# Optimization experiments

Measured on AMD Instinct MI355X. Metric: run time of the kernel, lower is better.

## Reference

```python
import jax, jax.numpy as jnp
import numpy as np
from jax.ops import segment_sum, segment_max

N_ROAD = 100000; E_ROAD = 400000
N_ZONE = 20000;  E_ZONE = 160000
D_ID = 64; D_ATTR = 16; H = 128; N_TYPES = 32


def setup_inputs():
    key = jax.random.key(0)
    ks = [jax.random.fold_in(key, i) for i in range(64)]
    it = iter(ks)
    p = lambda *s: jax.random.normal(next(it), s, jnp.float32) * 0.02
    inp = {
        'road_id_emb': p(N_ROAD, D_ID),
        'len_W': p(1, D_ATTR), 'len_b': p(D_ATTR),
        'type_emb': p(N_TYPES, D_ATTR),
        'lon_W': p(1, D_ATTR), 'lon_b': p(D_ATTR),
        'lat_W': p(1, D_ATTR), 'lat_b': p(D_ATTR),
        'road_attr_len': jax.random.normal(next(it), (N_ROAD,), jnp.float32),
        'road_attr_type': jax.random.randint(next(it), (N_ROAD,), 0, N_TYPES),
        'road_attr_lon': jax.random.normal(next(it), (N_ROAD,), jnp.float32),
        'road_attr_lat': jax.random.normal(next(it), (N_ROAD,), jnp.float32),
        'road_edge_index': jax.random.randint(next(it), (2, E_ROAD), 0, N_ROAD),
        'intersection_attr': jax.random.normal(next(it), (E_ROAD, 2), jnp.float32),
        'gat1_Wl': p(H, H), 'gat1_bl': p(H), 'gat1_Wr': p(H, H), 'gat1_br': p(H),
        'gat1_We': p(2, H), 'gat1_att': p(H), 'gat1_bias': p(H),
        'gat2_Wl': p(H, H), 'gat2_bl': p(H), 'gat2_Wr': p(H, H), 'gat2_br': p(H),
        'gat2_We': p(2, H), 'gat2_att': p(H), 'gat2_bias': p(H),
        'zone_id_emb': p(N_ZONE, H),
        'zone_edge_index': jax.random.randint(next(it), (2, E_ZONE), 0, N_ZONE),
        'zone_edge_weight': jax.random.uniform(next(it), (E_ZONE,), jnp.float32, 0.1, 1.0),
        'gcn1_W': p(H, H), 'gcn1_b': p(H),
        'gcn2_W': p(H, H), 'gcn2_b': p(H),
    }
    return inp


def gatv2_layer(x, src, dst, edge_attr, Wl, bl, Wr, br, We, att, bias):
    # GATv2Conv, heads=1, concat, negative_slope=0.2, add_self_loops with
    # fill_value='mean' for edge_attr (mean of incoming edge attrs per node).
    N = x.shape[0]
    ones = jnp.ones((src.shape[0],), x.dtype)
    cnt = segment_sum(ones, dst, num_segments=N)
    mean_ea = segment_sum(edge_attr, dst, num_segments=N) / jnp.maximum(cnt, 1.0)[:, None]
    loop = jnp.arange(N)
    src2 = jnp.concatenate([src, loop])
    dst2 = jnp.concatenate([dst, loop])
    ea2 = jnp.concatenate([edge_attr, mean_ea], axis=0)
    xl = x @ Wl + bl   # source transform (messages)
    xr = x @ Wr + br   # target transform
    e = jax.nn.leaky_relu(xl[src2] + xr[dst2] + ea2 @ We, 0.2)  # [E2, H]
    logits = e @ att  # [E2]
    m = jax.lax.stop_gradient(segment_max(logits, dst2, num_segments=N))
    ex = jnp.exp(logits - m[dst2])
    denom = segment_sum(ex, dst2, num_segments=N)
    alpha = ex / denom[dst2]
    out = segment_sum(alpha[:, None] * xl[src2], dst2, num_segments=N)
    return out + bias


def gcn_layer(x, src, dst, w, W, b):
    # GCNConv with add_self_loops (weight 1) and symmetric normalization.
    N = x.shape[0]
    loop = jnp.arange(N)
    src2 = jnp.concatenate([src, loop])
    dst2 = jnp.concatenate([dst, loop])
    w2 = jnp.concatenate([w, jnp.ones((N,), x.dtype)])
    deg = segment_sum(w2, dst2, num_segments=N)
    dinv = jnp.where(deg > 0, jax.lax.rsqrt(jnp.maximum(deg, 1e-12)), 0.0)
    norm = dinv[src2] * w2 * dinv[dst2]
    h = x @ W
    return segment_sum(norm[:, None] * h[src2], dst2, num_segments=N) + b


def reference(road_id_emb, len_W, len_b, type_emb, lon_W, lon_b, lat_W, lat_b,
              road_attr_len, road_attr_type, road_attr_lon, road_attr_lat,
              road_edge_index, intersection_attr,
              gat1_Wl, gat1_bl, gat1_Wr, gat1_br, gat1_We, gat1_att, gat1_bias,
              gat2_Wl, gat2_bl, gat2_Wr, gat2_br, gat2_We, gat2_att, gat2_bias,
              zone_id_emb, zone_edge_index, zone_edge_weight,
              gcn1_W, gcn1_b, gcn2_W, gcn2_b):
    # ---- road node features: id emb || len lin || type emb || lon lin || lat lin
    x = jnp.concatenate([
        road_id_emb,
        road_attr_len[:, None] @ len_W + len_b,
        type_emb[road_attr_type],
        road_attr_lon[:, None] @ lon_W + lon_b,
        road_attr_lat[:, None] @ lat_W + lat_b,
    ], axis=1)  # [N_ROAD, H]
    src, dst = road_edge_index[0], road_edge_index[1]
    h = jax.nn.relu(gatv2_layer(x, src, dst, intersection_attr,
                                gat1_Wl, gat1_bl, gat1_Wr, gat1_br, gat1_We, gat1_att, gat1_bias))
    road_out = gatv2_layer(h, src, dst, intersection_attr,
                           gat2_Wl, gat2_bl, gat2_Wr, gat2_br, gat2_We, gat2_att, gat2_bias)
    # ---- zone GCN over zone_id embedding table
    zsrc, zdst = zone_edge_index[0], zone_edge_index[1]
    zh = jax.nn.relu(gcn_layer(zone_id_emb, zsrc, zdst, zone_edge_weight, gcn1_W, gcn1_b))
    zone_out = gcn_layer(zh, zsrc, zdst, zone_edge_weight, gcn2_W, gcn2_b)
    return road_out, zone_out
```

## Files before the change

kernel.cpp:

```cpp
#include <hip/hip_runtime.h>
#include <math.h>


typedef __attribute__((ext_vector_type(8))) short bf16x8;
typedef __attribute__((ext_vector_type(4))) float f32x4;

static __device__ __forceinline__ unsigned short f2b(float f) {
  unsigned u = __float_as_uint(f);
  u = (u + 0x7FFFu + ((u >> 16) & 1u)) >> 16;
  return (unsigned short)u;
}
static __device__ __forceinline__ float b2f(unsigned short u) {
  return __uint_as_float(((unsigned)u) << 16);
}

__global__ __launch_bounds__(256) void wcast6(
    const float* __restrict__ W0, const float* __restrict__ W1, const float* __restrict__ W2,
    const float* __restrict__ W3, const float* __restrict__ W4, const float* __restrict__ W5,
    unsigned short* __restrict__ WT) {
  int b = blockIdx.x >> 6;
  int idx = (blockIdx.x & 63) * 256 + threadIdx.x;
  const float* W = (b == 0) ? W0 : (b == 1) ? W1 : (b == 2) ? W2 : (b == 3) ? W3 : (b == 4) ? W4 : W5;
  int n = idx >> 7, k = idx & 127;
  WT[b * 16384 + idx] = f2b(W[k * 128 + n]);
}


__global__ __launch_bounds__(256) void hist2(const int* __restrict__ dstR, int E,
                                             const int* __restrict__ dstZ, int EZ,
                                             int* __restrict__ histR, int* __restrict__ histZ) {
  int e = blockIdx.x * 256 + threadIdx.x;
  if (e < E) atomicAdd(histR + dstR[e], 1);
  else if (e - E < EZ) atomicAdd(histZ + dstZ[e - E], 1);
}

__global__ __launch_bounds__(256) void scan_local2(
    const int* __restrict__ inR, int* __restrict__ outR, int* __restrict__ bsumR, int nR, int nbR,
    const int* __restrict__ inZ, int* __restrict__ outZ, int* __restrict__ bsumZ, int nZ) {
  __shared__ int lds[256];
  const int* in; int* out; int* bsum; int n; int bid;
  if ((int)blockIdx.x < nbR) { in = inR; out = outR; bsum = bsumR; n = nR; bid = blockIdx.x; }
  else { in = inZ; out = outZ; bsum = bsumZ; n = nZ; bid = blockIdx.x - nbR; }
  int t = threadIdx.x;
  int base = bid * 1024 + t * 4;
  int v0 = base + 0 < n ? in[base + 0] : 0;
  int v1 = base + 1 < n ? in[base + 1] : 0;
  int v2 = base + 2 < n ? in[base + 2] : 0;
  int v3 = base + 3 < n ? in[base + 3] : 0;
  int s = v0 + v1 + v2 + v3;
  lds[t] = s;
  __syncthreads();
  for (int off = 1; off < 256; off <<= 1) {
    int x = (t >= off) ? lds[t - off] : 0;
    __syncthreads();
    if (t >= off) lds[t] += x;
    __syncthreads();
  }
  int excl = lds[t] - s;
  if (t == 255) bsum[bid] = lds[255];
  if (base + 0 < n) out[base + 0] = excl;
  if (base + 1 < n) out[base + 1] = excl + v0;
  if (base + 2 < n) out[base + 2] = excl + v0 + v1;
  if (base + 3 < n) out[base + 3] = excl + v0 + v1 + v2;
}

__global__ __launch_bounds__(256) void scan_bsum2(int* __restrict__ bsumR, int nbR,
                                                  int* __restrict__ bsumZ, int nbZ) {
  __shared__ int lds[256];
  int* bsum = blockIdx.x ? bsumZ : bsumR;
  int nb = blockIdx.x ? nbZ : nbR;
  int t = threadIdx.x;
  int v = (t < nb) ? bsum[t] : 0;
  lds[t] = v;
  __syncthreads();
  for (int off = 1; off < 256; off <<= 1) {
    int x = (t >= off) ? lds[t - off] : 0;
    __syncthreads();
    if (t >= off) lds[t] += x;
    __syncthreads();
  }
  if (t < nb) bsum[t] = lds[t] - v;
}

__global__ __launch_bounds__(256) void scan_add2(int* __restrict__ outR, const int* __restrict__ bsumR, int nR,
                                                 int* __restrict__ outZ, const int* __restrict__ bsumZ, int nZ) {
  int i = blockIdx.x * 256 + threadIdx.x;
  if (i < nR) outR[i] += bsumR[i >> 10];
  else if (i - nR < nZ) { int j = i - nR; outZ[j] += bsumZ[j >> 10]; }
}

__global__ __launch_bounds__(256) void scatter2(
    const int* __restrict__ srcR, const int* __restrict__ dstR, const float* __restrict__ ia,
    const int* __restrict__ rowstart, int* __restrict__ cursor,
    int* __restrict__ csr_src, float2* __restrict__ csr_ea, int E,
    const int* __restrict__ srcZ, const int* __restrict__ dstZ, const float* __restrict__ zw,
    const int* __restrict__ zrowstart, int* __restrict__ zcursor,
    int* __restrict__ zcsr_src, float* __restrict__ zcsr_w, int EZ) {
  int e = blockIdx.x * 256 + threadIdx.x;
  if (e < E) {
    int d = dstR[e];
    int idx = rowstart[d] + atomicAdd(cursor + d, 1);
    csr_src[idx] = srcR[e];
    csr_ea[idx] = make_float2(ia[2 * e], ia[2 * e + 1]);
  } else if (e - E < EZ) {
    int ez = e - E;
    int d = dstZ[ez];
    int idx = zrowstart[d] + atomicAdd(zcursor + d, 1);
    zcsr_src[idx] = srcZ[ez];
    zcsr_w[idx] = zw[ez];
  }
}

__global__ __launch_bounds__(256) void meanea_dinv_k(
    const int* __restrict__ rowstart, const int* __restrict__ hist,
    const float2* __restrict__ csr_ea, float2* __restrict__ mea, int N,
    const int* __restrict__ zrowstart, const int* __restrict__ zhist,
    const float* __restrict__ zcsr_w, float* __restrict__ dinv, int NZ) {
  int i = blockIdx.x * 256 + threadIdx.x;
  if (i < N) {
    int st = rowstart[i], deg = hist[i];
    float a = 0.f, b = 0.f;
    for (int k = 0; k < deg; ++k) {
      float2 v = csr_ea[st + k];
      a += v.x; b += v.y;
    }
    float c = deg > 0 ? 1.f / (float)deg : 0.f;
    mea[i] = make_float2(a * c, b * c);
  } else if (i - N < NZ) {
    int d = i - N;
    int st = zrowstart[d], deg = zhist[d];
    float s = 1.f;
    for (int k = 0; k < deg; ++k) s += zcsr_w[st + k];
    dinv[d] = rsqrtf(s);
  }
}

template <int DUAL>
__device__ __forceinline__ void gemm_core(
    unsigned short (*Xs)[136],
    const unsigned short* __restrict__ WlT, const unsigned short* __restrict__ WrT,
    const float* __restrict__ bl, const float* __restrict__ br,
    unsigned short* __restrict__ Yl, unsigned short* __restrict__ Yr,
    int row0, int N) {
  constexpr int MT = DUAL ? 4 : 2;
  int t = threadIdx.x;
  int w = t >> 6, lane = t & 63;
  int mb = DUAL ? 0 : (w >> 1) * 2;
  int ncol0 = (w & 1) * 64;
  const bool isR = DUAL && (w >> 1);
  const unsigned short* WTw = isR ? WrT : WlT;
  const float* bias = isR ? br : bl;
  int l15 = lane & 15, l4 = lane >> 4;

  bf16x8 b0[4], b1[4];
#pragma unroll
  for (int nt = 0; nt < 4; ++nt) {
    const unsigned short* p = WTw + (size_t)(ncol0 + nt * 16 + l15) * 128 + l4 * 8;
    b0[nt] = *reinterpret_cast<const bf16x8*>(p);
  }
  f32x4 acc[MT][4];
#pragma unroll
  for (int mt = 0; mt < MT; ++mt)
#pragma unroll
    for (int nt = 0; nt < 4; ++nt)
      acc[mt][nt] = (f32x4){0.f, 0.f, 0.f, 0.f};

#pragma unroll
  for (int ks = 0; ks < 4; ++ks) {
    bf16x8* bc = (ks & 1) ? b1 : b0;
    bf16x8* bn = (ks & 1) ? b0 : b1;
    if (ks < 3) {
#pragma unroll
      for (int nt = 0; nt < 4; ++nt) {
        const unsigned short* p = WTw + (size_t)(ncol0 + nt * 16 + l15) * 128 + (ks + 1) * 32 + l4 * 8;
        bn[nt] = *reinterpret_cast<const bf16x8*>(p);
      }
    }
    bf16x8 a[MT];
#pragma unroll
    for (int mt = 0; mt < MT; ++mt)
      a[mt] = *reinterpret_cast<const bf16x8*>(&Xs[(mb + mt) * 16 + l15][ks * 32 + l4 * 8]);
#pragma unroll
    for (int mt = 0; mt < MT; ++mt)
#pragma unroll
      for (int nt = 0; nt < 4; ++nt)
        acc[mt][nt] = __builtin_amdgcn_mfma_f32_16x16x32_bf16(bc[nt], a[mt], acc[mt][nt], 0, 0, 0);
  }

  const int passes = DUAL ? 2 : 1;
#pragma unroll
  for (int pass = 0; pass < passes; ++pass) {
    __syncthreads();
    if (!DUAL || (w >> 1) == pass) {
#pragma unroll
      for (int nt = 0; nt < 4; ++nt) {
        int c0 = ncol0 + nt * 16 + l4 * 4;
        float4 bv = make_float4(0.f, 0.f, 0.f, 0.f);
        if (bias) bv = *reinterpret_cast<const float4*>(bias + c0);
#pragma unroll
        for (int mt = 0; mt < MT; ++mt) {
          int rl = (mb + mt) * 16 + l15;
          ushort4 pk;
          pk.x = f2b(acc[mt][nt][0] + bv.x);
          pk.y = f2b(acc[mt][nt][1] + bv.y);
          pk.z = f2b(acc[mt][nt][2] + bv.z);
          pk.w = f2b(acc[mt][nt][3] + bv.w);
          *reinterpret_cast<ushort4*>(&Xs[rl][c0]) = pk;
        }
      }
    }
    __syncthreads();
    unsigned short* Yt = DUAL ? (pass ? Yr : Yl) : Yl;
#pragma unroll
    for (int q = 0; q < 4; ++q) {
      int lin = q * 256 + t;
      int r = lin >> 4, cc = (lin & 15) * 8;
      int row = row0 + r;
      if (row < N)
        *reinterpret_cast<bf16x8*>(Yt + (size_t)row * 128 + cc) =
            *reinterpret_cast<const bf16x8*>(&Xs[r][cc]);
    }
  }
}

template <int DUAL, int XBF>
__global__ __launch_bounds__(256) void gemm_mfma(
    const void* __restrict__ Xv,
    const unsigned short* __restrict__ WlT, const unsigned short* __restrict__ WrT,
    const float* __restrict__ bl, const float* __restrict__ br,
    unsigned short* __restrict__ Yl, unsigned short* __restrict__ Yr, int N) {
  __shared__ __align__(16) unsigned short Xs[64][136];
  int t = threadIdx.x;
  int row0 = blockIdx.x * 64;
  if (XBF) {
    const unsigned short* Xb = (const unsigned short*)Xv;
#pragma unroll
    for (int q = 0; q < 8; ++q) {
      int lin = q * 256 + t;
      int r = lin >> 5, kf = (lin & 31) * 4;
      int row = min(row0 + r, N - 1);
      *reinterpret_cast<ushort4*>(&Xs[r][kf]) =
          *reinterpret_cast<const ushort4*>(Xb + (size_t)row * 128 + kf);
    }
  } else {
    const float* Xf = (const float*)Xv;
#pragma unroll
    for (int q = 0; q < 8; ++q) {
      int lin = q * 256 + t;
      int r = lin >> 5, kf = (lin & 31) * 4;
      int row = min(row0 + r, N - 1);
      float4 xv = *reinterpret_cast<const float4*>(Xf + (size_t)row * 128 + kf);
      ushort4 pk;
      pk.x = f2b(xv.x); pk.y = f2b(xv.y); pk.z = f2b(xv.z); pk.w = f2b(xv.w);
      *reinterpret_cast<ushort4*>(&Xs[r][kf]) = pk;
    }
  }
  __syncthreads();
  gemm_core<DUAL>(Xs, WlT, WrT, bl, br, Yl, Yr, row0, N);
}

__global__ __launch_bounds__(256) void feat_gemm1(
    const float* __restrict__ id_emb, const float* __restrict__ lenW, const float* __restrict__ lenb,
    const float* __restrict__ type_emb, const float* __restrict__ lonW, const float* __restrict__ lonb,
    const float* __restrict__ latW, const float* __restrict__ latb,
    const float* __restrict__ alen, const int* __restrict__ atype,
    const float* __restrict__ alon, const float* __restrict__ alat,
    const unsigned short* __restrict__ WlT, const unsigned short* __restrict__ WrT,
    const float* __restrict__ bl, const float* __restrict__ br,
    unsigned short* __restrict__ Yl, unsigned short* __restrict__ Yr, int N) {
  __shared__ __align__(16) unsigned short Xs[64][136];
  int t = threadIdx.x;
  int row0 = blockIdx.x * 64;
#pragma unroll
  for (int q = 0; q < 8; ++q) {
    int lin = q * 256 + t;
    int r = lin >> 5, kf = (lin & 31) * 4;
    int row = min(row0 + r, N - 1);
    float v0, v1, v2, v3;
    if (kf < 64) {
      float4 e = *reinterpret_cast<const float4*>(id_emb + (size_t)row * 64 + kf);
      v0 = e.x; v1 = e.y; v2 = e.z; v3 = e.w;
    } else if (kf < 80) {
      float a = alen[row]; int j = kf - 64;
      v0 = a * lenW[j] + lenb[j]; v1 = a * lenW[j + 1] + lenb[j + 1];
      v2 = a * lenW[j + 2] + lenb[j + 2]; v3 = a * lenW[j + 3] + lenb[j + 3];
    } else if (kf < 96) {
      int ty = atype[row];
      float4 e = *reinterpret_cast<const float4*>(type_emb + ty * 16 + (kf - 80));
      v0 = e.x; v1 = e.y; v2 = e.z; v3 = e.w;
    } else if (kf < 112) {
      float a = alon[row]; int j = kf - 96;
      v0 = a * lonW[j] + lonb[j]; v1 = a * lonW[j + 1] + lonb[j + 1];
      v2 = a * lonW[j + 2] + lonb[j + 2]; v3 = a * lonW[j + 3] + lonb[j + 3];
    } else {
      float a = alat[row]; int j = kf - 112;
      v0 = a * latW[j] + latb[j]; v1 = a * latW[j + 1] + latb[j + 1];
      v2 = a * latW[j + 2] + latb[j + 2]; v3 = a * latW[j + 3] + latb[j + 3];
    }
    ushort4 pk;
    pk.x = f2b(v0); pk.y = f2b(v1); pk.z = f2b(v2); pk.w = f2b(v3);
    *reinterpret_cast<ushort4*>(&Xs[r][kf]) = pk;
  }
  __syncthreads();
  gemm_core<1>(Xs, WlT, WrT, bl, br, Yl, Yr, row0, N);
}

__device__ __forceinline__ float4 gat_one(
    const unsigned short* __restrict__ xl, float4 xr4,
    int d, int st, int deg, float2 me, int lane,
    const int* __restrict__ csr_src, const float2* __restrict__ csr_ea,
    float4 w0, float4 w1, float4 at) {
  float denom;
  float4 acc;
  {
    ushort4 av = *reinterpret_cast<const ushort4*>(xl + (size_t)d * 128 + lane * 4);
    float4 a;
    a.x = b2f(av.x); a.y = b2f(av.y); a.z = b2f(av.z); a.w = b2f(av.w);
    float4 v;
    v.x = a.x + xr4.x + me.x * w0.x + me.y * w1.x; v.x = v.x > 0.f ? v.x : 0.2f * v.x;
    v.y = a.y + xr4.y + me.x * w0.y + me.y * w1.y; v.y = v.y > 0.f ? v.y : 0.2f * v.y;
    v.z = a.z + xr4.z + me.x * w0.z + me.y * w1.z; v.z = v.z > 0.f ? v.z : 0.2f * v.z;
    v.w = a.w + xr4.w + me.x * w0.w + me.y * w1.w; v.w = v.w > 0.f ? v.w : 0.2f * v.w;
    float p = v.x * at.x + v.y * at.y + v.z * at.z + v.w * at.w;
#pragma unroll
    for (int off = 16; off; off >>= 1) p += __shfl_xor(p, off, 32);
    float wgt = __expf(p);
    denom = wgt;
    acc.x = wgt * a.x; acc.y = wgt * a.y; acc.z = wgt * a.z; acc.w = wgt * a.w;
  }
  for (int base = 0; base < deg; base += 32) {
    int rem = deg - base;
    int chunk = rem < 32 ? rem : 32;
    int k = st + base + lane;
    int sidx = 0;
    float2 eav = make_float2(0.f, 0.f);
    if (lane < chunk) { sidx = csr_src[k]; eav = csr_ea[k]; }
    auto edge = [&](ushort4 avv, int i) {
      float ea0 = __shfl(eav.x, i, 32);
      float ea1 = __shfl(eav.y, i, 32);
      float4 a;
      a.x = b2f(avv.x); a.y = b2f(avv.y); a.z = b2f(avv.z); a.w = b2f(avv.w);
      float4 v;
      v.x = a.x + xr4.x + ea0 * w0.x + ea1 * w1.x; v.x = v.x > 0.f ? v.x : 0.2f * v.x;
      v.y = a.y + xr4.y + ea0 * w0.y + ea1 * w1.y; v.y = v.y > 0.f ? v.y : 0.2f * v.y;
      v.z = a.z + xr4.z + ea0 * w0.z + ea1 * w1.z; v.z = v.z > 0.f ? v.z : 0.2f * v.z;
      v.w = a.w + xr4.w + ea0 * w0.w + ea1 * w1.w; v.w = v.w > 0.f ? v.w : 0.2f * v.w;
      float p = v.x * at.x + v.y * at.y + v.z * at.z + v.w * at.w;
#pragma unroll
      for (int off = 16; off; off >>= 1) p += __shfl_xor(p, off, 32);
      float wgt = __expf(p);
      denom += wgt;
      acc.x += wgt * a.x; acc.y += wgt * a.y; acc.z += wgt * a.z; acc.w += wgt * a.w;
    };
    for (int i0 = 0; i0 < chunk; i0 += 4) {
      int cnt = chunk - i0; if (cnt > 4) cnt = 4;
      int s0 = __shfl(sidx, i0 + 0, 32);
      int s1 = __shfl(sidx, i0 + 1, 32);
      int s2 = __shfl(sidx, i0 + 2, 32);
      int s3 = __shfl(sidx, i0 + 3, 32);
      ushort4 a0, a1, a2, a3;
      a0 = *reinterpret_cast<const ushort4*>(xl + (size_t)s0 * 128 + lane * 4);
      if (cnt > 1) a1 = *reinterpret_cast<const ushort4*>(xl + (size_t)s1 * 128 + lane * 4);
      if (cnt > 2) a2 = *reinterpret_cast<const ushort4*>(xl + (size_t)s2 * 128 + lane * 4);
      if (cnt > 3) a3 = *reinterpret_cast<const ushort4*>(xl + (size_t)s3 * 128 + lane * 4);
      edge(a0, i0 + 0);
      if (cnt > 1) edge(a1, i0 + 1);
      if (cnt > 2) edge(a2, i0 + 2);
      if (cnt > 3) edge(a3, i0 + 3);
    }
  }
  float inv = 1.f / denom;
  float4 o;
  o.x = acc.x * inv; o.y = acc.y * inv; o.z = acc.z * inv; o.w = acc.w * inv;
  return o;
}

template <int OUTBF>
__global__ __launch_bounds__(256) void gat_node(
    const unsigned short* __restrict__ xl, const unsigned short* __restrict__ xr,
    const int* __restrict__ rowstart, const int* __restrict__ hist,
    const int* __restrict__ csr_src, const float2* __restrict__ csr_ea,
    const float2* __restrict__ mean_ea,
    const float* __restrict__ We, const float* __restrict__ att, const float* __restrict__ bias,
    void* __restrict__ out, int N, int relu) {
  __shared__ float sW0[128], sW1[128], sAtt[128], sBias[128];
  int t = threadIdx.x;
  if (t < 128) { sW0[t] = We[t]; sW1[t] = We[128 + t]; }
  else { int j = t - 128; sAtt[j] = att[j]; sBias[j] = bias[j]; }
  __syncthreads();
  int grp = t >> 5, lane = t & 31;
  int d = blockIdx.x * 8 + grp;
  if (d >= N) return;
  float4 w0 = *reinterpret_cast<const float4*>(sW0 + lane * 4);
  float4 w1 = *reinterpret_cast<const float4*>(sW1 + lane * 4);
  float4 at = *reinterpret_cast<const float4*>(sAtt + lane * 4);
  float4 bv = *reinterpret_cast<const float4*>(sBias + lane * 4);
  ushort4 xrv = *reinterpret_cast<const ushort4*>(xr + (size_t)d * 128 + lane * 4);
  float4 xr4;
  xr4.x = b2f(xrv.x); xr4.y = b2f(xrv.y); xr4.z = b2f(xrv.z); xr4.w = b2f(xrv.w);
  float4 o = gat_one(xl, xr4, d, rowstart[d], hist[d], mean_ea[d], lane,
                     csr_src, csr_ea, w0, w1, at);
  o.x += bv.x; o.y += bv.y; o.z += bv.z; o.w += bv.w;
  if (relu) {
    o.x = fmaxf(o.x, 0.f); o.y = fmaxf(o.y, 0.f);
    o.z = fmaxf(o.z, 0.f); o.w = fmaxf(o.w, 0.f);
  }
  if (OUTBF) {
    ushort4 p4;
    p4.x = f2b(o.x); p4.y = f2b(o.y); p4.z = f2b(o.z); p4.w = f2b(o.w);
    *reinterpret_cast<ushort4*>((unsigned short*)out + (size_t)d * 128 + lane * 4) = p4;
  } else {
    *reinterpret_cast<float4*>((float*)out + (size_t)d * 128 + lane * 4) = o;
  }
}

__device__ __forceinline__ float4 gcn_one(
    const unsigned short* __restrict__ h, int d, int st, int deg, float dv, int lane,
    const int* __restrict__ csr_src, const float* __restrict__ csr_w,
    const float* __restrict__ dinv) {
  ushort4 hv = *reinterpret_cast<const ushort4*>(h + (size_t)d * 128 + lane * 4);
  float dv2 = dv * dv;
  float4 acc;
  acc.x = dv2 * b2f(hv.x); acc.y = dv2 * b2f(hv.y);
  acc.z = dv2 * b2f(hv.z); acc.w = dv2 * b2f(hv.w);
  for (int base = 0; base < deg; base += 32) {
    int rem = deg - base;
    int chunk = rem < 32 ? rem : 32;
    int k = st + base + lane;
    int sidx = 0;
    float wv = 0.f, dvs = 0.f;
    if (lane < chunk) {
      sidx = csr_src[k];
      wv = csr_w[k];
      dvs = dinv[sidx];
    }
    auto edge = [&](ushort4 avv, int i) {
      float coef = __shfl(dvs, i, 32) * __shfl(wv, i, 32) * dv;
      acc.x += coef * b2f(avv.x); acc.y += coef * b2f(avv.y);
      acc.z += coef * b2f(avv.z); acc.w += coef * b2f(avv.w);
    };
    for (int i0 = 0; i0 < chunk; i0 += 4) {
      int cnt = chunk - i0; if (cnt > 4) cnt = 4;
      int s0 = __shfl(sidx, i0 + 0, 32);
      int s1 = __shfl(sidx, i0 + 1, 32);
      int s2 = __shfl(sidx, i0 + 2, 32);
      int s3 = __shfl(sidx, i0 + 3, 32);
      ushort4 a0, a1, a2, a3;
      a0 = *reinterpret_cast<const ushort4*>(h + (size_t)s0 * 128 + lane * 4);
      if (cnt > 1) a1 = *reinterpret_cast<const ushort4*>(h + (size_t)s1 * 128 + lane * 4);
      if (cnt > 2) a2 = *reinterpret_cast<const ushort4*>(h + (size_t)s2 * 128 + lane * 4);
      if (cnt > 3) a3 = *reinterpret_cast<const ushort4*>(h + (size_t)s3 * 128 + lane * 4);
      edge(a0, i0 + 0);
      if (cnt > 1) edge(a1, i0 + 1);
      if (cnt > 2) edge(a2, i0 + 2);
      if (cnt > 3) edge(a3, i0 + 3);
    }
  }
  return acc;
}

template <int OUTBF>
__global__ __launch_bounds__(256) void gcn_node(const unsigned short* __restrict__ h,
                                                const int* __restrict__ rowstart,
                                                const int* __restrict__ hist, const int* __restrict__ csr_src,
                                                const float* __restrict__ csr_w, const float* __restrict__ dinv,
                                                const float* __restrict__ bias, void* __restrict__ out,
                                                int NZ, int relu) {
  int t = threadIdx.x, grp = t >> 5, lane = t & 31;
  int d = blockIdx.x * 8 + grp;
  if (d >= NZ) return;
  float4 acc = gcn_one(h, d, rowstart[d], hist[d], dinv[d], lane, csr_src, csr_w, dinv);
  float4 bv = *reinterpret_cast<const float4*>(bias + lane * 4);
  float4 o;
  o.x = acc.x + bv.x; o.y = acc.y + bv.y; o.z = acc.z + bv.z; o.w = acc.w + bv.w;
  if (relu) {
    o.x = fmaxf(o.x, 0.f); o.y = fmaxf(o.y, 0.f);
    o.z = fmaxf(o.z, 0.f); o.w = fmaxf(o.w, 0.f);
  }
  if (OUTBF) {
    ushort4 p4;
    p4.x = f2b(o.x); p4.y = f2b(o.y); p4.z = f2b(o.z); p4.w = f2b(o.w);
    *reinterpret_cast<ushort4*>((unsigned short*)out + (size_t)d * 128 + lane * 4) = p4;
  } else {
    *reinterpret_cast<float4*>((float*)out + (size_t)d * 128 + lane * 4) = o;
  }
}

extern "C" void kernel_launch(void* const* d_in, const int* in_sizes, int n_in,
                              void* d_out, int out_size, void* d_ws, size_t ws_size,
                              hipStream_t stream) {
  const float* road_id_emb = (const float*)d_in[0];
  const float* len_W = (const float*)d_in[1];
  const float* len_b = (const float*)d_in[2];
  const float* type_emb = (const float*)d_in[3];
  const float* lon_W = (const float*)d_in[4];
  const float* lon_b = (const float*)d_in[5];
  const float* lat_W = (const float*)d_in[6];
  const float* lat_b = (const float*)d_in[7];
  const float* alen = (const float*)d_in[8];
  const int* atype = (const int*)d_in[9];
  const float* alon = (const float*)d_in[10];
  const float* alat = (const float*)d_in[11];
  const int* rei = (const int*)d_in[12];
  const float* ia = (const float*)d_in[13];
  const float* zone_emb = (const float*)d_in[28];
  const int* zei = (const int*)d_in[29];
  const float* zw = (const float*)d_in[30];
  const float* gcn1_W = (const float*)d_in[31];
  const float* gcn1_b = (const float*)d_in[32];
  const float* gcn2_W = (const float*)d_in[33];
  const float* gcn2_b = (const float*)d_in[34];

  const int N = in_sizes[8];
  const int E = in_sizes[12] / 2;
  const int NZ = in_sizes[28] / 128;
  const int EZ = in_sizes[30];

  const int* src = rei;
  const int* dst = rei + E;
  const int* zsrc = zei;
  const int* zdst = zei + EZ;

  char* wp = (char*)d_ws;
  auto carve = [&](size_t bytes) {
    void* r = wp;
    wp += (bytes + 255) & ~(size_t)255;
    return r;
  };
  unsigned short* XRbf = (unsigned short*)carve((size_t)N * 128 * 2);
  unsigned short* Abf = (unsigned short*)carve((size_t)N * 128 * 2);
  unsigned short* Bbf = (unsigned short*)carve((size_t)N * 128 * 2);
  unsigned short* Cbf = (unsigned short*)carve((size_t)N * 128 * 2);
  float2* mean_ea = (float2*)carve((size_t)N * 8);
  int* rowstart = (int*)carve((size_t)N * 4);
  int* zrowstart = (int*)carve((size_t)NZ * 4);
  int* hist = (int*)carve((size_t)N * 4);
  int* cursor = (int*)carve((size_t)N * 4);
  int* zhist = (int*)carve((size_t)NZ * 4);
  int* zcursor = (int*)carve((size_t)NZ * 4);
  int* csr_src = (int*)carve((size_t)E * 4);
  float2* csr_ea = (float2*)carve((size_t)E * 8);
  int* bsumR = (int*)carve(1024);
  int* bsumZ = (int*)carve(1024);
  int* zcsr_src = (int*)carve((size_t)EZ * 4);
  float* zcsr_w = (float*)carve((size_t)EZ * 4);
  float* dinv = (float*)carve((size_t)NZ * 4);
  unsigned short* WT = (unsigned short*)carve(6 * 16384 * 2);
  unsigned short* WT0 = WT;
  unsigned short* WT1 = WT + 16384;
  unsigned short* WT2 = WT + 2 * 16384;
  unsigned short* WT3 = WT + 3 * 16384;
  unsigned short* WT4 = WT + 4 * 16384;
  unsigned short* WT5 = WT + 5 * 16384;

  float* road_out = (float*)d_out;
  float* zone_out = road_out + (size_t)N * 128;

  wcast6<<<384, 256, 0, stream>>>(
      (const float*)d_in[14], (const float*)d_in[16], (const float*)d_in[21],
      (const float*)d_in[23], gcn1_W, gcn2_W, WT);

  const int nbR = (N + 1023) / 1024;
  const int nbZ = (NZ + 1023) / 1024;
  hipMemsetAsync(hist, 0, (size_t)((char*)(zcursor + NZ) - (char*)hist), stream);
  hist2<<<(E + EZ + 255) / 256, 256, 0, stream>>>(dst, E, zdst, EZ, hist, zhist);
  scan_local2<<<nbR + nbZ, 256, 0, stream>>>(hist, rowstart, bsumR, N, nbR, zhist, zrowstart, bsumZ, NZ);
  scan_bsum2<<<2, 256, 0, stream>>>(bsumR, nbR, bsumZ, nbZ);
  scan_add2<<<(N + NZ + 255) / 256, 256, 0, stream>>>(rowstart, bsumR, N, zrowstart, bsumZ, NZ);
  scatter2<<<(E + EZ + 255) / 256, 256, 0, stream>>>(
      src, dst, ia, rowstart, cursor, csr_src, csr_ea, E,
      zsrc, zdst, zw, zrowstart, zcursor, zcsr_src, zcsr_w, EZ);
  meanea_dinv_k<<<(N + NZ + 255) / 256, 256, 0, stream>>>(
      rowstart, hist, csr_ea, mean_ea, N, zrowstart, zhist, zcsr_w, dinv, NZ);

  const int gemm_grid = (N + 63) / 64;
  const int node_grid = (N + 7) / 8;

  feat_gemm1<<<gemm_grid, 256, 0, stream>>>(
      road_id_emb, len_W, len_b, type_emb, lon_W, lon_b, lat_W, lat_b,
      alen, atype, alon, alat,
      WT0, WT1, (const float*)d_in[15], (const float*)d_in[17], Cbf, XRbf, N);
  gat_node<1><<<node_grid, 256, 0, stream>>>(
      Cbf, XRbf, rowstart, hist, csr_src, csr_ea, mean_ea,
      (const float*)d_in[18], (const float*)d_in[19], (const float*)d_in[20], Bbf, N, 1);
  gemm_mfma<1, 1><<<gemm_grid, 256, 0, stream>>>(
      Bbf, WT2, WT3, (const float*)d_in[22], (const float*)d_in[24], Cbf, Abf, N);
  gat_node<0><<<node_grid, 256, 0, stream>>>(
      Cbf, Abf, rowstart, hist, csr_src, csr_ea, mean_ea,
      (const float*)d_in[25], (const float*)d_in[26], (const float*)d_in[27], road_out, N, 0);

  unsigned short* HGbf = XRbf;
  unsigned short* ZAbf = XRbf + (size_t)NZ * 128;
  const int zgrid = (NZ + 63) / 64;
  const int znode_grid = (NZ + 7) / 8;
  gemm_mfma<0, 0><<<zgrid, 256, 0, stream>>>(zone_emb, WT4, nullptr, nullptr, nullptr, HGbf, nullptr, NZ);
  gcn_node<1><<<znode_grid, 256, 0, stream>>>(HGbf, zrowstart, zhist, zcsr_src, zcsr_w, dinv, gcn1_b, ZAbf, NZ, 1);
  gemm_mfma<0, 1><<<zgrid, 256, 0, stream>>>(ZAbf, WT5, nullptr, nullptr, nullptr, HGbf, nullptr, NZ);
  gcn_node<0><<<znode_grid, 256, 0, stream>>>(HGbf, zrowstart, zhist, zcsr_src, zcsr_w, dinv, gcn2_b, zone_out, NZ, 0);
}
```

Baseline: 283.5 us.

## Fold attribute linear layers and type embedding into precomputed first GAT projection

Precomputes the contributions of the len/lon/lat linear features, the 32 type embeddings and the biases through the first GATv2 Wl/Wr weights. The first-layer GEMM then runs only over the 64-wide id embedding (K=64) and adds the folded rank-1 terms and the type-table row in the epilogue. This halves the MFMA K dimension and removes the per-element attribute feature construction. It changes rounding, because the attribute path now stays in fp32 instead of passing through bf16 inputs, and it adds one tiny extra kernel.

```diff
diff --git a/kernel.cpp b/kernel.cpp
--- a/kernel.cpp
+++ b/kernel.cpp
@@ -23,6 +23,42 @@
   const float* W = (b == 0) ? W0 : (b == 1) ? W1 : (b == 2) ? W2 : (b == 3) ? W3 : (b == 4) ? W4 : W5;
   int n = idx >> 7, k = idx & 127;
   WT[b * 16384 + idx] = f2b(W[k * 128 + n]);
+}
+
+__global__ __launch_bounds__(128) void feat_fold(
+    const float* __restrict__ Wl, const float* __restrict__ blv,
+    const float* __restrict__ Wr, const float* __restrict__ brv,
+    const float* __restrict__ lenW, const float* __restrict__ lenb,
+    const float* __restrict__ type_emb,
+    const float* __restrict__ lonW, const float* __restrict__ lonb,
+    const float* __restrict__ latW, const float* __restrict__ latb,
+    float* __restrict__ FL) {
+  int b = blockIdx.x;
+  int mat = b / 36, r = b % 36;
+  int n = threadIdx.x;
+  const float* W = mat ? Wr : Wl;
+  const float* bias = mat ? brv : blv;
+  float s = 0.f;
+  if (r < 32) {
+#pragma unroll
+    for (int j = 0; j < 16; ++j) s += type_emb[r * 16 + j] * W[(80 + j) * 128 + n];
+  } else if (r == 32) {
+#pragma unroll
+    for (int j = 0; j < 16; ++j) s += lenW[j] * W[(64 + j) * 128 + n];
+  } else if (r == 33) {
+#pragma unroll
+    for (int j = 0; j < 16; ++j) s += lonW[j] * W[(96 + j) * 128 + n];
+  } else if (r == 34) {
+#pragma unroll
+    for (int j = 0; j < 16; ++j) s += latW[j] * W[(112 + j) * 128 + n];
+  } else {
+    s = bias[n];
+#pragma unroll
+    for (int j = 0; j < 16; ++j)
+      s += lenb[j] * W[(64 + j) * 128 + n] + lonb[j] * W[(96 + j) * 128 + n] +
+           latb[j] * W[(112 + j) * 128 + n];
+  }
+  FL[(mat * 36 + r) * 128 + n] = s;
 }
 
 
@@ -260,49 +296,107 @@
 }
 
 __global__ __launch_bounds__(256) void feat_gemm1(
-    const float* __restrict__ id_emb, const float* __restrict__ lenW, const float* __restrict__ lenb,
-    const float* __restrict__ type_emb, const float* __restrict__ lonW, const float* __restrict__ lonb,
-    const float* __restrict__ latW, const float* __restrict__ latb,
+    const float* __restrict__ id_emb,
     const float* __restrict__ alen, const int* __restrict__ atype,
     const float* __restrict__ alon, const float* __restrict__ alat,
     const unsigned short* __restrict__ WlT, const unsigned short* __restrict__ WrT,
-    const float* __restrict__ bl, const float* __restrict__ br,
+    const float* __restrict__ FLl, const float* __restrict__ FLr,
     unsigned short* __restrict__ Yl, unsigned short* __restrict__ Yr, int N) {
   __shared__ __align__(16) unsigned short Xs[64][136];
   int t = threadIdx.x;
   int row0 = blockIdx.x * 64;
-#pragma unroll
-  for (int q = 0; q < 8; ++q) {
+  int w = t >> 6, lane = t & 63;
+  int ncol0 = (w & 1) * 64;
+  const bool isR = (w >> 1);
+  const unsigned short* WTw = isR ? WrT : WlT;
+  const float* FL = isR ? FLr : FLl;
+  int l15 = lane & 15, l4 = lane >> 4;
+
+  bf16x8 b0[4], b1[4];
+#pragma unroll
+  for (int nt = 0; nt < 4; ++nt) {
+    const unsigned short* p = WTw + (size_t)(ncol0 + nt * 16 + l15) * 128 + l4 * 8;
+    b0[nt] = *reinterpret_cast<const bf16x8*>(p);
+    b1[nt] = *reinterpret_cast<const bf16x8*>(p + 32);
+  }
+
+#pragma unroll
+  for (int q = 0; q < 4; ++q) {
     int lin = q * 256 + t;
-    int r = lin >> 5, kf = (lin & 31) * 4;
+    int r = lin >> 4, kf = (lin & 15) * 4;
     int row = min(row0 + r, N - 1);
-    float v0, v1, v2, v3;
-    if (kf < 64) {
-      float4 e = *reinterpret_cast<const float4*>(id_emb + (size_t)row * 64 + kf);
-      v0 = e.x; v1 = e.y; v2 = e.z; v3 = e.w;
-    } else if (kf < 80) {
-      float a = alen[row]; int j = kf - 64;
-      v0 = a * lenW[j] + lenb[j]; v1 = a * lenW[j + 1] + lenb[j + 1];
-      v2 = a * lenW[j + 2] + lenb[j + 2]; v3 = a * lenW[j + 3] + lenb[j + 3];
-    } else if (kf < 96) {
-      int ty = atype[row];
-      float4 e = *reinterpret_cast<const float4*>(type_emb + ty * 16 + (kf - 80));
-      v0 = e.x; v1 = e.y; v2 = e.z; v3 = e.w;
-    } else if (kf < 112) {
-      float a = alon[row]; int j = kf - 96;
-      v0 = a * lonW[j] + lonb[j]; v1 = a * lonW[j + 1] + lonb[j + 1];
-      v2 = a * lonW[j + 2] + lonb[j + 2]; v3 = a * lonW[j + 3] + lonb[j + 3];
-    } else {
-      float a = alat[row]; int j = kf - 112;
-      v0 = a * latW[j] + latb[j]; v1 = a * latW[j + 1] + latb[j + 1];
-      v2 = a * latW[j + 2] + latb[j + 2]; v3 = a * latW[j + 3] + latb[j + 3];
-    }
+    float4 xv = *reinterpret_cast<const float4*>(id_emb + (size_t)row * 64 + kf);
     ushort4 pk;
-    pk.x = f2b(v0); pk.y = f2b(v1); pk.z = f2b(v2); pk.w = f2b(v3);
+    pk.x = f2b(xv.x); pk.y = f2b(xv.y); pk.z = f2b(xv.z); pk.w = f2b(xv.w);
     *reinterpret_cast<ushort4*>(&Xs[r][kf]) = pk;
   }
   __syncthreads();
-  gemm_core<1>(Xs, WlT, WrT, bl, br, Yl, Yr, row0, N);
+
+  f32x4 acc[4][4];
+#pragma unroll
+  for (int mt = 0; mt < 4; ++mt)
+#pragma unroll
+    for (int nt = 0; nt < 4; ++nt)
+      acc[mt][nt] = (f32x4){0.f, 0.f, 0.f, 0.f};
+
+#pragma unroll
+  for (int ks = 0; ks < 2; ++ks) {
+    bf16x8* bc = ks ? b1 : b0;
+    bf16x8 a[4];
+#pragma unroll
+    for (int mt = 0; mt < 4; ++mt)
+      a[mt] = *reinterpret_cast<const bf16x8*>(&Xs[mt * 16 + l15][ks * 32 + l4 * 8]);
+#pragma unroll
+    for (int mt = 0; mt < 4; ++mt)
+#pragma unroll
+      for (int nt = 0; nt < 4; ++nt)
+        acc[mt][nt] = __builtin_amdgcn_mfma_f32_16x16x32_bf16(bc[nt], a[mt], acc[mt][nt], 0, 0, 0);
+  }
+
+  float lenv[4], lonv[4], latv[4];
+  int tyv[4];
+#pragma unroll
+  for (int mt = 0; mt < 4; ++mt) {
+    int row = min(row0 + mt * 16 + l15, N - 1);
+    lenv[mt] = alen[row]; lonv[mt] = alon[row]; latv[mt] = alat[row];
+    tyv[mt] = atype[row];
+  }
+
+#pragma unroll
+  for (int pass = 0; pass < 2; ++pass) {
+    __syncthreads();
+    if ((int)isR == pass) {
+#pragma unroll
+      for (int nt = 0; nt < 4; ++nt) {
+        int c0 = ncol0 + nt * 16 + l4 * 4;
+        float4 vl = *reinterpret_cast<const float4*>(FL + 32 * 128 + c0);
+        float4 vo = *reinterpret_cast<const float4*>(FL + 33 * 128 + c0);
+        float4 va = *reinterpret_cast<const float4*>(FL + 34 * 128 + c0);
+        float4 vc = *reinterpret_cast<const float4*>(FL + 35 * 128 + c0);
+#pragma unroll
+        for (int mt = 0; mt < 4; ++mt) {
+          float4 tv = *reinterpret_cast<const float4*>(FL + tyv[mt] * 128 + c0);
+          ushort4 pk;
+          pk.x = f2b(acc[mt][nt][0] + lenv[mt] * vl.x + lonv[mt] * vo.x + latv[mt] * va.x + tv.x + vc.x);
+          pk.y = f2b(acc[mt][nt][1] + lenv[mt] * vl.y + lonv[mt] * vo.y + latv[mt] * va.y + tv.y + vc.y);
+          pk.z = f2b(acc[mt][nt][2] + lenv[mt] * vl.z + lonv[mt] * vo.z + latv[mt] * va.z + tv.z + vc.z);
+          pk.w = f2b(acc[mt][nt][3] + lenv[mt] * vl.w + lonv[mt] * vo.w + latv[mt] * va.w + tv.w + vc.w);
+          *reinterpret_cast<ushort4*>(&Xs[mt * 16 + l15][c0]) = pk;
+        }
+      }
+    }
+    __syncthreads();
+    unsigned short* Yt = pass ? Yr : Yl;
+#pragma unroll
+    for (int q = 0; q < 4; ++q) {
+      int lin = q * 256 + t;
+      int r = lin >> 4, cc = (lin & 15) * 8;
+      int row = row0 + r;
+      if (row < N)
+        *reinterpret_cast<bf16x8*>(Yt + (size_t)row * 128 + cc) =
+            *reinterpret_cast<const bf16x8*>(&Xs[r][cc]);
+    }
+  }
 }
 
 __device__ __forceinline__ float4 gat_one(
@@ -546,12 +640,15 @@
   float* zcsr_w = (float*)carve((size_t)EZ * 4);
   float* dinv = (float*)carve((size_t)NZ * 4);
   unsigned short* WT = (unsigned short*)carve(6 * 16384 * 2);
+  float* FL = (float*)carve(2 * 36 * 128 * 4);
   unsigned short* WT0 = WT;
   unsigned short* WT1 = WT + 16384;
   unsigned short* WT2 = WT + 2 * 16384;
   unsigned short* WT3 = WT + 3 * 16384;
   unsigned short* WT4 = WT + 4 * 16384;
   unsigned short* WT5 = WT + 5 * 16384;
+  float* FLl = FL;
+  float* FLr = FL + 36 * 128;
 
   float* road_out = (float*)d_out;
   float* zone_out = road_out + (size_t)N * 128;
@@ -559,6 +656,10 @@
   wcast6<<<384, 256, 0, stream>>>(
       (const float*)d_in[14], (const float*)d_in[16], (const float*)d_in[21],
       (const float*)d_in[23], gcn1_W, gcn2_W, WT);
+  feat_fold<<<72, 128, 0, stream>>>(
+      (const float*)d_in[14], (const float*)d_in[15],
+      (const float*)d_in[16], (const float*)d_in[17],
+      len_W, len_b, type_emb, lon_W, lon_b, lat_W, lat_b, FL);
 
   const int nbR = (N + 1023) / 1024;
   const int nbZ = (NZ + 1023) / 1024;
@@ -577,9 +678,8 @@
   const int node_grid = (N + 7) / 8;
 
   feat_gemm1<<<gemm_grid, 256, 0, stream>>>(
-      road_id_emb, len_W, len_b, type_emb, lon_W, lon_b, lat_W, lat_b,
-      alen, atype, alon, alat,
-      WT0, WT1, (const float*)d_in[15], (const float*)d_in[17], Cbf, XRbf, N);
+      road_id_emb, alen, atype, alon, alat,
+      WT0, WT1, FLl, FLr, Cbf, XRbf, N);
   gat_node<1><<<node_grid, 256, 0, stream>>>(
       Cbf, XRbf, rowstart, hist, csr_src, csr_ea, mean_ea,
       (const float*)d_in[18], (const float*)d_in[19], (const float*)d_in[20], Bbf, N, 1);
```

Result: faster. 267.7 us (-5.6%).
